# Kernel optimization log

Measured on AMD Instinct MI355X. Metric: run time of the kernel, lower is better.

The kernel has to match this reference:

```python
import jax, jax.numpy as jnp
import numpy as np

N = 128       # SSM state size
L = 32768     # l_max / sequence length
DT_MIN, DT_MAX = 0.001, 0.1


def setup_inputs() -> dict:
    key = jax.random.key(0)
    ku, ka, kb, kc, ks = jax.random.split(key, 5)
    u = jax.random.normal(ku, (L,), dtype=jnp.float32)
    # lecun_normal: std = 1/sqrt(fan_in); shift A by -2I for stability over L powers
    A = jax.random.normal(ka, (N, N), dtype=jnp.float32) * (1.0 / np.sqrt(N)) - 2.0 * jnp.eye(N, dtype=jnp.float32)
    B = jax.random.normal(kb, (N, 1), dtype=jnp.float32)            # fan_in=1 -> std 1
    C = jax.random.normal(kc, (1, N), dtype=jnp.float32) * (1.0 / np.sqrt(N))
    D = jnp.ones((1,), dtype=jnp.float32)
    log_step = jax.random.uniform(ks, (1,), dtype=jnp.float32) * (np.log(DT_MAX) - np.log(DT_MIN)) + np.log(DT_MIN)
    return {"u": u, "A": A, "B": B, "C": C, "D": D, "log_step": log_step}


def discretize(a, b, step):
    # bilinear (Tustin) discretization, identical to the flax module
    i = jnp.eye(a.shape[0], dtype=a.dtype)
    bl = jnp.linalg.inv(i - (step / 2.0) * a)
    ab = bl @ (i + (step / 2.0) * a)
    bb = (bl * step) @ b
    return ab, bb


def k_conv(ab, bb, cb, l):
    # K[t] = cb @ ab^t @ bb  -- same math as the matrix_power list-comp,
    # computed with a single scan carrying x_t = ab^t @ bb  (N,1)
    def step(x, _):
        k_t = (cb @ x).reshape(())
        return ab @ x, k_t
    _, k = jax.lax.scan(step, bb, None, length=l)
    return k  # (l,)


def causal_convolution(u, k):
    l = u.shape[0]
    ud = jnp.fft.rfft(jnp.pad(u, (0, k.shape[0])))
    kd = jnp.fft.rfft(jnp.pad(k, (0, l)))
    return jnp.fft.irfft(ud * kd)[:l]


def reference(u, A, B, C, D, log_step):
    step = jnp.exp(log_step)
    ab, bb = discretize(A, B, step)
    K = k_conv(ab, bb, C, u.shape[0])
    return causal_convolution(u, K) + D * u
```

## Files before the change

### kernel.cpp

```cpp
#include <hip/hip_runtime.h>
#include <math.h>

#define L_SEQ 32768
#define RSTR 136
#define PL   17408
#define GP   16384

typedef unsigned short u16;
typedef float f32x4 __attribute__((ext_vector_type(4)));
typedef short bf16x8 __attribute__((ext_vector_type(8)));
typedef u16 u16x4 __attribute__((ext_vector_type(4)));

__device__ __forceinline__ u16 f2bf(float x) {
  unsigned u = __float_as_uint(x);
  u = u + 0x7FFFu + ((u >> 16) & 1u);
  return (u16)(u >> 16);
}
__device__ __forceinline__ float bf2f(u16 h) {
  return __uint_as_float(((unsigned)h) << 16);
}
__device__ __forceinline__ int sg(int k) {
  return (k & 7) + ((k >> 5) << 3) + (((k >> 3) & 3) << 5);
}
__device__ __forceinline__ f32x4 MF(bf16x8 a, bf16x8 b, f32x4 c) {
  return __builtin_amdgcn_mfma_f32_16x16x32_bf16(a, b, c, 0, 0, 0);
}

template<int ASRC,int BSRC,int OUTM,int OUTG,int MODE>
__device__ void mm(u16* lds, const u16* gA, int aPl, const u16* gB, int bPl,
                   u16* gO, int oPl, int gOrow0, u16* gO2,
                   int Mrows, int N, float c3, const u16* gE, const u16* gEt) {
  u16* Mh = lds;          u16* Ml = lds + PL;
  u16* Th = lds + 2 * PL; u16* Tl = lds + 3 * PL;
  const int t = threadIdx.x, lane = t & 63;
  const int la = lane & 15, g = lane >> 4;
  const int w = t >> 6;
  const int r0 = (w >> 2) << 5, c0 = (w & 3) << 5;
  constexpr bool doA = (OUTM == 2) || (OUTG == 2) || (OUTG == 3);
  constexpr bool doT = (OUTM >= 1) || (OUTG == 1) || (OUTG == 3);
  const bool act = (r0 < Mrows) && (c0 < N);

  __syncthreads();

  f32x4 acc[2][2], accT[2][2];
#pragma unroll
  for (int i = 0; i < 2; ++i)
#pragma unroll
    for (int j = 0; j < 2; ++j) {
      acc[i][j] = (f32x4){0.f, 0.f, 0.f, 0.f};
      accT[i][j] = (f32x4){0.f, 0.f, 0.f, 0.f};
    }

  if (act) {
#pragma unroll
    for (int kb = 0; kb < 4; ++kb) {
      const int kp = (g << 5) + (kb << 3);
      bf16x8 Ah[2], Al[2], Bh[2], Bl[2];
#pragma unroll
      for (int fr = 0; fr < 2; ++fr) {
        const int ar = r0 + (fr << 4) + la;
        if constexpr (ASRC == 0) {
          Ah[fr] = *(const bf16x8*)(Mh + ar * RSTR + kp);
          Al[fr] = *(const bf16x8*)(Ml + ar * RSTR + kp);
        } else {
          Ah[fr] = *(const bf16x8*)(gA + ar * 128 + kp);
          Al[fr] = *(const bf16x8*)(gA + aPl + ar * 128 + kp);
        }
      }
#pragma unroll
      for (int fc = 0; fc < 2; ++fc) {
        const int bc = c0 + (fc << 4) + la;
        if constexpr (BSRC == 0) {
          Bh[fc] = *(const bf16x8*)(Th + bc * RSTR + kp);
          Bl[fc] = *(const bf16x8*)(Tl + bc * RSTR + kp);
        } else {
          Bh[fc] = *(const bf16x8*)(gB + bc * 128 + kp);
          Bl[fc] = *(const bf16x8*)(gB + bPl + bc * 128 + kp);
        }
      }
#pragma unroll
      for (int fr = 0; fr < 2; ++fr)
#pragma unroll
        for (int fc = 0; fc < 2; ++fc) {
          if constexpr (doA) {
            acc[fr][fc] = MF(Ah[fr], Bh[fc], acc[fr][fc]);
            acc[fr][fc] = MF(Ah[fr], Bl[fc], acc[fr][fc]);
            acc[fr][fc] = MF(Al[fr], Bh[fc], acc[fr][fc]);
          }
          if constexpr (doT) {
            accT[fr][fc] = MF(Bh[fc], Ah[fr], accT[fr][fc]);
            accT[fr][fc] = MF(Bh[fc], Al[fr], accT[fr][fc]);
            accT[fr][fc] = MF(Bl[fc], Ah[fr], accT[fr][fc]);
          }
        }
    }
  }

  __syncthreads();

  if (!act) return;

  if constexpr (doT) {
#pragma unroll
    for (int fr = 0; fr < 2; ++fr)
#pragma unroll
      for (int fc = 0; fc < 2; ++fc) {
        const int rr = r0 + (fr << 4) + la;
        const int cb = c0 + (fc << 4) + (g << 2);
        const int scb = sg(cb);
        float v[4];
#pragma unroll
        for (int j = 0; j < 4; ++j) v[j] = accT[fr][fc][j];
        if constexpr (MODE == 2) {
#pragma unroll
          for (int j = 0; j < 4; ++j)
            v[j] += bf2f(gE[rr * 128 + scb + j]) + bf2f(gE[GP + rr * 128 + scb + j])
                  + bf2f(Mh[rr * RSTR + scb + j]) + bf2f(Ml[rr * RSTR + scb + j])
                  + ((rr == cb + j) ? 1.f : 0.f);
        }
        if constexpr (MODE == 4) {
#pragma unroll
          for (int j = 0; j < 4; ++j)
            v[j] = c3 * (v[j] + bf2f(gE[rr * 128 + scb + j]) +
                         bf2f(gE[GP + rr * 128 + scb + j])) -
                   ((rr == cb + j) ? 1.f : 0.f);
        }
        u16x4 hi, lo;
#pragma unroll
        for (int j = 0; j < 4; ++j) {
          u16 h = f2bf(v[j]); hi[j] = h; lo[j] = f2bf(v[j] - bf2f(h));
        }
        if constexpr (OUTM == 2) {
          *(u16x4*)(Mh + rr * RSTR + scb) = hi;
          *(u16x4*)(Ml + rr * RSTR + scb) = lo;
        }
        if constexpr (OUTG == 1) {
          if (rr < Mrows) {
            *(u16x4*)(gO + (gOrow0 + rr) * 128 + scb) = hi;
            *(u16x4*)(gO + oPl + (gOrow0 + rr) * 128 + scb) = lo;
          }
        }
        if constexpr (OUTG == 3) {
          *(u16x4*)(gO + rr * 128 + scb) = hi;
          *(u16x4*)(gO + oPl + rr * 128 + scb) = lo;
        }
      }
  }
  if constexpr (doA) {
#pragma unroll
    for (int fr = 0; fr < 2; ++fr)
#pragma unroll
      for (int fc = 0; fc < 2; ++fc) {
        const int cc = c0 + (fc << 4) + la;
        const int rb = r0 + (fr << 4) + (g << 2);
        const int srb = sg(rb);
        float v[4];
#pragma unroll
        for (int j = 0; j < 4; ++j) v[j] = acc[fr][fc][j];
        if constexpr (MODE == 2) {
          const int scc = sg(cc);
#pragma unroll
          for (int j = 0; j < 4; ++j)
            v[j] += bf2f(gE[(rb + j) * 128 + scc]) + bf2f(gE[GP + (rb + j) * 128 + scc])
                  + bf2f(Th[cc * RSTR + srb + j]) + bf2f(Tl[cc * RSTR + srb + j])
                  + ((rb + j == cc) ? 1.f : 0.f);
        }
        if constexpr (MODE == 4) {
#pragma unroll
          for (int j = 0; j < 4; ++j)
            v[j] = c3 * (v[j] + bf2f(gEt[cc * 128 + srb + j]) +
                         bf2f(gEt[GP + cc * 128 + srb + j])) -
                   ((rb + j == cc) ? 1.f : 0.f);
        }
        u16x4 hi, lo;
#pragma unroll
        for (int j = 0; j < 4; ++j) {
          u16 h = f2bf(v[j]); hi[j] = h; lo[j] = f2bf(v[j] - bf2f(h));
        }
        if constexpr (OUTM == 2) {
          *(u16x4*)(Th + cc * RSTR + srb) = hi;
          *(u16x4*)(Tl + cc * RSTR + srb) = lo;
        }
        if constexpr (OUTG == 2) {
          if (cc < N) {
            *(u16x4*)(gO + (gOrow0 + cc) * 128 + srb) = hi;
            *(u16x4*)(gO + oPl + (gOrow0 + cc) * 128 + srb) = lo;
          }
        }
        if constexpr (OUTG == 3) {
          *(u16x4*)(gO2 + cc * 128 + srb) = hi;
          *(u16x4*)(gO2 + oPl + cc * 128 + srb) = lo;
        }
      }
  }
}

__global__ void __launch_bounds__(1024, 4) chain_k(const float* __restrict__ A,
                                                   const float* __restrict__ Bv,
                                                   const float* __restrict__ Cv,
                                                   const float* __restrict__ lstep,
                                                   u16* ws) {
  extern __shared__ u16 lds[];
  const int bid = blockIdx.x;
  u16* gT    = ws + bid * 131072;
  u16* gU12  = gT + 32768;
  u16* gU12t = gT + 65536;
  u16* rt = ws + 262144;
  u16* gs = ws + 327680;

  const int t = threadIdx.x;
  const float step = expf(lstep[0]);
  const float alpha = 0.5f * step / (1.f + step);
  const float c3 = 2.f / (1.f + step);
  u16* Mh = lds; u16* Ml = lds + PL; u16* Th = lds + 2 * PL; u16* Tl = lds + 3 * PL;

#pragma unroll
  for (int i = 0; i < 4; ++i) {
    int e4 = (t + (i << 10)) << 2;
    int r = e4 >> 7, c = e4 & 127;
    float4 av = *(const float4*)(A + e4);
    float vv[4] = {av.x, av.y, av.z, av.w};
    u16x4 hi, lo;
#pragma unroll
    for (int j = 0; j < 4; ++j) {
      float v = alpha * (vv[j] + ((r == c + j) ? 2.f : 0.f));
      u16 h = f2bf(v); hi[j] = h; lo[j] = f2bf(v - bf2f(h));
    }
    int sc = sg(c), sr = sg(r);
    *(u16x4*)(Mh + r * RSTR + sc) = hi;
    *(u16x4*)(Ml + r * RSTR + sc) = lo;
    *(u16x4*)(gT + r * 128 + sc) = hi;
    *(u16x4*)(gT + GP + r * 128 + sc) = lo;
#pragma unroll
    for (int j = 0; j < 4; ++j) {
      Th[(c + j) * RSTR + sr] = hi[j];
      Tl[(c + j) * RSTR + sr] = lo[j];
    }
  }

  mm<0,0,2,0,0>(lds, 0,0, 0,0, 0,0,0,0, 128,128, 0.f, 0,0);
  mm<1,0,0,3,2>(lds, gT,GP, 0,0, gU12,GP,0,gU12t, 128,128, 0.f, gT,0);
  mm<0,0,2,0,0>(lds, 0,0, 0,0, 0,0,0,0, 128,128, 0.f, 0,0);
  mm<1,0,2,0,4>(lds, gU12,GP, 0,0, 0,0,0,0, 128,128, c3, gU12,gU12t);

  if (bid == 0) {
    __syncthreads();
    if (t < 128) {
      float a2 = 0.f;
      for (int p = 0; p < 128; ++p)
        a2 = fmaf(bf2f(Mh[t * RSTR + p]) + bf2f(Ml[t * RSTR + p]), Bv[sg(p)], a2);
      float v = 0.5f * step * (a2 + Bv[t]);
      u16 h = f2bf(v);
      rt[sg(t)] = h;
      rt[32768 + sg(t)] = f2bf(v - bf2f(h));
    }
    for (int k = 0; k < 8; ++k) {
      mm<0,1,0,2,0>(lds, 0,0, rt,32768, rt,32768,(1<<k),0, 128,(1<<k), 0.f, 0,0);
      if (k < 7) mm<0,0,2,0,0>(lds, 0,0, 0,0, 0,0,0,0, 128,128, 0.f, 0,0);
    }
  } else {
    __syncthreads();
    if (t < 128) {
      float v = Cv[t];
      u16 h = f2bf(v);
      gs[sg(t)] = h;
      gs[GP + sg(t)] = f2bf(v - bf2f(h));
    }
    for (int k = 0; k < 8; ++k)
      mm<0,0,2,0,0>(lds, 0,0, 0,0, 0,0,0,0, 128,128, 0.f, 0,0);
    for (int k = 0; k < 7; ++k) {
      mm<1,0,0,1,0>(lds, gs,GP, 0,0, gs,GP,(1<<k),0, (1<<k),128, 0.f, 0,0);
      if (k < 6) mm<0,0,2,0,0>(lds, 0,0, 0,0, 0,0,0,0, 128,128, 0.f, 0,0);
    }
  }
}

__global__ __launch_bounds__(256) void kmat_k(const u16* __restrict__ gs,
                                              const u16* __restrict__ rt,
                                              float* __restrict__ Kv) {
  __shared__ float srow[128];
  int t1 = blockIdx.x, t0 = threadIdx.x;
  if (t0 < 128)
    srow[t0] = bf2f(gs[t1 * 128 + t0]) + bf2f(gs[GP + t1 * 128 + t0]);
  __syncthreads();
  const u16* rh = rt + t0 * 128;
  const u16* rl = rt + 32768 + t0 * 128;
  float acc = 0.f;
#pragma unroll 4
  for (int p = 0; p < 128; p += 8) {
    uint4 qh = *(const uint4*)(rh + p);
    uint4 ql = *(const uint4*)(rl + p);
    unsigned dh[4] = {qh.x, qh.y, qh.z, qh.w};
    unsigned dl[4] = {ql.x, ql.y, ql.z, ql.w};
#pragma unroll
    for (int j = 0; j < 4; ++j) {
      acc = fmaf(srow[p + 2 * j],     bf2f((u16)dh[j]) + bf2f((u16)dl[j]), acc);
      acc = fmaf(srow[p + 2 * j + 1],
                 bf2f((u16)(dh[j] >> 16)) + bf2f((u16)(dl[j] >> 16)), acc);
    }
  }
  Kv[t1 * 256 + t0] = acc;
}

__global__ __launch_bounds__(128) void conv_k(const float* __restrict__ u,
                                              const float* __restrict__ Kv,
                                              float* __restrict__ Pp) {
  __shared__ __align__(16) float ks[512];
  __shared__ __align__(16) float usw[1024];

  int bid = blockIdx.x, tid = threadIdx.x;
  int m = (int)((sqrtf(8.f * (float)bid + 1.f) - 1.f) * 0.5f);
  while ((m + 1) * (m + 2) / 2 <= bid) ++m;
  while (m * (m + 1) / 2 > bid) --m;
  int c = bid - m * (m + 1) / 2;
  int w0 = (m - c - 1) << 9;

  for (int idx = tid; idx < 512; idx += 128) ks[idx] = Kv[(c << 9) + idx];
  for (int idx = tid; idx < 1024; idx += 128) {
    int gi = w0 + idx;
    float v = (gi >= 0) ? u[gi] : 0.f;
    int b = idx >> 2;
    int pb = b ^ ((b >> 3) & 7);
    usw[(pb << 2) | (idx & 3)] = v;
  }
  __syncthreads();

  int tb = tid << 2;

#define LD4(x)                                                      \
  (*(const float4*)&usw[((((x) >> 2) ^ ((((x) >> 2) >> 3) & 7)) << 2)])

  float4 wlo = LD4(508 + tb);
  float4 whi = LD4(512 + tb);
  float acc0 = 0.f, acc1 = 0.f, acc2 = 0.f, acc3 = 0.f;

#pragma unroll 4
  for (int s8 = 0; s8 < 512; s8 += 4) {
    float4 k4 = *(const float4*)&ks[s8];
    acc0 = fmaf(k4.x, whi.x, acc0);
    acc0 = fmaf(k4.y, wlo.w, acc0);
    acc0 = fmaf(k4.z, wlo.z, acc0);
    acc0 = fmaf(k4.w, wlo.y, acc0);
    acc1 = fmaf(k4.x, whi.y, acc1);
    acc1 = fmaf(k4.y, whi.x, acc1);
    acc1 = fmaf(k4.z, wlo.w, acc1);
    acc1 = fmaf(k4.w, wlo.z, acc1);
    acc2 = fmaf(k4.x, whi.z, acc2);
    acc2 = fmaf(k4.y, whi.y, acc2);
    acc2 = fmaf(k4.z, whi.x, acc2);
    acc2 = fmaf(k4.w, wlo.w, acc2);
    acc3 = fmaf(k4.x, whi.w, acc3);
    acc3 = fmaf(k4.y, whi.z, acc3);
    acc3 = fmaf(k4.z, whi.y, acc3);
    acc3 = fmaf(k4.w, whi.x, acc3);
    if (s8 < 508) {
      whi = wlo;
      wlo = LD4(504 + tb - s8);
    }
  }
#undef LD4

  float* dst = Pp + (bid << 9) + tb;
  *(float4*)dst = make_float4(acc0, acc1, acc2, acc3);
}

__global__ __launch_bounds__(256) void reduce_k(const float* __restrict__ Pp,
                                                const float* __restrict__ u,
                                                const float* __restrict__ D,
                                                float* __restrict__ y) {
  int t = blockIdx.x * 256 + threadIdx.x;
  if (t >= L_SEQ) return;
  int m = t >> 9;
  int base = ((m * (m + 1) / 2) << 9) + (t & 511);
  float acc = D[0] * u[t];
  for (int c = 0; c <= m; ++c) acc += Pp[base + (c << 9)];
  y[t] = acc;
}

extern "C" void kernel_launch(void* const* d_in, const int* in_sizes, int n_in,
                              void* d_out, int out_size, void* d_ws, size_t ws_size,
                              hipStream_t stream) {
  (void)in_sizes; (void)n_in; (void)out_size; (void)ws_size;
  const float* u     = (const float*)d_in[0];
  const float* A     = (const float*)d_in[1];
  const float* B     = (const float*)d_in[2];
  const float* C     = (const float*)d_in[3];
  const float* D     = (const float*)d_in[4];
  const float* lstep = (const float*)d_in[5];
  float* y = (float*)d_out;
  u16* ws = (u16*)d_ws;

  u16* rt = ws + 262144;
  u16* gs = ws + 327680;
  float* Kv = (float*)((char*)d_ws + 720896);
  float* Pp = (float*)((char*)d_ws + 851968);

  (void)hipFuncSetAttribute((const void*)chain_k,
                            hipFuncAttributeMaxDynamicSharedMemorySize, 139264);
  hipLaunchKernelGGL(chain_k, dim3(2), dim3(1024), 139264, stream, A, B, C, lstep, ws);
  hipLaunchKernelGGL(kmat_k, dim3(128), dim3(256), 0, stream, gs, rt, Kv);
  hipLaunchKernelGGL(conv_k, dim3(2080), dim3(128), 0, stream, u, Kv, Pp);
  hipLaunchKernelGGL(reduce_k, dim3(L_SEQ / 256), dim3(256), 0, stream, Pp, u, D, y);
}
```

Baseline: 210.2 us.

## Swizzle LDS matrix layout, double-buffer MFMA operand loads, drop redundant barriers

The padded, k-permuted LDS layout (stride 136 with the sg permutation) is replaced by an unpadded 128-stride layout with an XOR swizzle, so the global buffers now use natural ordering and the LDS footprint shrinks. The K-loop now prefetches the next k-block's operand fragments into a second register set while the current MFMAs run. The post-accumulation barrier is skipped when the result is not written back to LDS. These target LDS bank conflicts and latency in the serial matrix-squaring chain, at the cost of more registers and a change to the k-index mapping that every consumer must match.

```diff
diff --git a/kernel.cpp b/kernel.cpp
--- a/kernel.cpp
+++ b/kernel.cpp
@@ -2,9 +2,8 @@
 #include <math.h>
 
 #define L_SEQ 32768
-#define RSTR 136
-#define PL   17408
-#define GP   16384
+#define PL 16384
+#define GP 16384
 
 typedef unsigned short u16;
 typedef float f32x4 __attribute__((ext_vector_type(4)));
@@ -19,8 +18,8 @@
 __device__ __forceinline__ float bf2f(u16 h) {
   return __uint_as_float(((unsigned)h) << 16);
 }
-__device__ __forceinline__ int sg(int k) {
-  return (k & 7) + ((k >> 5) << 3) + (((k >> 3) & 3) << 5);
+__device__ __forceinline__ int MIDX(int r, int c) {
+  return (r << 7) + (c ^ ((r & 7) << 3));
 }
 __device__ __forceinline__ f32x4 MF(bf16x8 a, bf16x8 b, f32x4 c) {
   return __builtin_amdgcn_mfma_f32_16x16x32_bf16(a, b, c, 0, 0, 0);
@@ -37,7 +36,7 @@
   const int w = t >> 6;
   const int r0 = (w >> 2) << 5, c0 = (w & 3) << 5;
   constexpr bool doA = (OUTM == 2) || (OUTG == 2) || (OUTG == 3);
-  constexpr bool doT = (OUTM >= 1) || (OUTG == 1) || (OUTG == 3);
+  constexpr bool doT = (OUTM == 2) || (OUTG == 1) || (OUTG == 3);
   const bool act = (r0 < Mrows) && (c0 < N);
 
   __syncthreads();
@@ -52,51 +51,56 @@
     }
 
   if (act) {
-#pragma unroll
-    for (int kb = 0; kb < 4; ++kb) {
-      const int kp = (g << 5) + (kb << 3);
-      bf16x8 Ah[2], Al[2], Bh[2], Bl[2];
+    bf16x8 Ah[2][2], Al[2][2], Bh[2][2], Bl[2][2];
+    auto load_stage = [&](int kb, int s) {
+      const int kp = (kb << 5) + (g << 3);
 #pragma unroll
       for (int fr = 0; fr < 2; ++fr) {
         const int ar = r0 + (fr << 4) + la;
         if constexpr (ASRC == 0) {
-          Ah[fr] = *(const bf16x8*)(Mh + ar * RSTR + kp);
-          Al[fr] = *(const bf16x8*)(Ml + ar * RSTR + kp);
+          Ah[s][fr] = *(const bf16x8*)(Mh + MIDX(ar, kp));
+          Al[s][fr] = *(const bf16x8*)(Ml + MIDX(ar, kp));
         } else {
-          Ah[fr] = *(const bf16x8*)(gA + ar * 128 + kp);
-          Al[fr] = *(const bf16x8*)(gA + aPl + ar * 128 + kp);
+          Ah[s][fr] = *(const bf16x8*)(gA + ar * 128 + kp);
+          Al[s][fr] = *(const bf16x8*)(gA + aPl + ar * 128 + kp);
         }
       }
 #pragma unroll
       for (int fc = 0; fc < 2; ++fc) {
         const int bc = c0 + (fc << 4) + la;
         if constexpr (BSRC == 0) {
-          Bh[fc] = *(const bf16x8*)(Th + bc * RSTR + kp);
-          Bl[fc] = *(const bf16x8*)(Tl + bc * RSTR + kp);
+          Bh[s][fc] = *(const bf16x8*)(Th + MIDX(bc, kp));
+          Bl[s][fc] = *(const bf16x8*)(Tl + MIDX(bc, kp));
         } else {
-          Bh[fc] = *(const bf16x8*)(gB + bc * 128 + kp);
-          Bl[fc] = *(const bf16x8*)(gB + bPl + bc * 128 + kp);
+          Bh[s][fc] = *(const bf16x8*)(gB + bc * 128 + kp);
+          Bl[s][fc] = *(const bf16x8*)(gB + bPl + bc * 128 + kp);
         }
       }
+    };
+    load_stage(0, 0);
+#pragma unroll
+    for (int kb = 0; kb < 4; ++kb) {
+      const int cur = kb & 1;
+      if (kb < 3) load_stage(kb + 1, cur ^ 1);
 #pragma unroll
       for (int fr = 0; fr < 2; ++fr)
 #pragma unroll
         for (int fc = 0; fc < 2; ++fc) {
           if constexpr (doA) {
-            acc[fr][fc] = MF(Ah[fr], Bh[fc], acc[fr][fc]);
-            acc[fr][fc] = MF(Ah[fr], Bl[fc], acc[fr][fc]);
-            acc[fr][fc] = MF(Al[fr], Bh[fc], acc[fr][fc]);
+            acc[fr][fc] = MF(Ah[cur][fr], Bh[cur][fc], acc[fr][fc]);
+            acc[fr][fc] = MF(Ah[cur][fr], Bl[cur][fc], acc[fr][fc]);
+            acc[fr][fc] = MF(Al[cur][fr], Bh[cur][fc], acc[fr][fc]);
           }
           if constexpr (doT) {
-            accT[fr][fc] = MF(Bh[fc], Ah[fr], accT[fr][fc]);
-            accT[fr][fc] = MF(Bh[fc], Al[fr], accT[fr][fc]);
-            accT[fr][fc] = MF(Bl[fc], Ah[fr], accT[fr][fc]);
+            accT[fr][fc] = MF(Bh[cur][fc], Ah[cur][fr], accT[fr][fc]);
+            accT[fr][fc] = MF(Bh[cur][fc], Al[cur][fr], accT[fr][fc]);
+            accT[fr][fc] = MF(Bl[cur][fc], Ah[cur][fr], accT[fr][fc]);
           }
         }
     }
   }
 
-  __syncthreads();
+  if constexpr (OUTM == 2) __syncthreads();
 
   if (!act) return;
 
@@ -107,22 +111,21 @@
       for (int fc = 0; fc < 2; ++fc) {
         const int rr = r0 + (fr << 4) + la;
         const int cb = c0 + (fc << 4) + (g << 2);
-        const int scb = sg(cb);
         float v[4];
 #pragma unroll
         for (int j = 0; j < 4; ++j) v[j] = accT[fr][fc][j];
         if constexpr (MODE == 2) {
 #pragma unroll
           for (int j = 0; j < 4; ++j)
-            v[j] += bf2f(gE[rr * 128 + scb + j]) + bf2f(gE[GP + rr * 128 + scb + j])
-                  + bf2f(Mh[rr * RSTR + scb + j]) + bf2f(Ml[rr * RSTR + scb + j])
+            v[j] += bf2f(gE[rr * 128 + cb + j]) + bf2f(gE[GP + rr * 128 + cb + j])
+                  + bf2f(Mh[MIDX(rr, cb + j)]) + bf2f(Ml[MIDX(rr, cb + j)])
                   + ((rr == cb + j) ? 1.f : 0.f);
         }
         if constexpr (MODE == 4) {
 #pragma unroll
           for (int j = 0; j < 4; ++j)
-            v[j] = c3 * (v[j] + bf2f(gE[rr * 128 + scb + j]) +
-                         bf2f(gE[GP + rr * 128 + scb + j])) -
+            v[j] = c3 * (v[j] + bf2f(gE[rr * 128 + cb + j]) +
+                         bf2f(gE[GP + rr * 128 + cb + j])) -
                    ((rr == cb + j) ? 1.f : 0.f);
         }
         u16x4 hi, lo;
@@ -131,18 +134,18 @@
           u16 h = f2bf(v[j]); hi[j] = h; lo[j] = f2bf(v[j] - bf2f(h));
         }
         if constexpr (OUTM == 2) {
-          *(u16x4*)(Mh + rr * RSTR + scb) = hi;
-          *(u16x4*)(Ml + rr * RSTR + scb) = lo;
+          *(u16x4*)(Mh + MIDX(rr, cb)) = hi;
+          *(u16x4*)(Ml + MIDX(rr, cb)) = lo;
         }
         if constexpr (OUTG == 1) {
           if (rr < Mrows) {
-            *(u16x4*)(gO + (gOrow0 + rr) * 128 + scb) = hi;
-            *(u16x4*)(gO + oPl + (gOrow0 + rr) * 128 + scb) = lo;
+            *(u16x4*)(gO + (gOrow0 + rr) * 128 + cb) = hi;
+            *(u16x4*)(gO + oPl + (gOrow0 + rr) * 128 + cb) = lo;
           }
         }
         if constexpr (OUTG == 3) {
-          *(u16x4*)(gO + rr * 128 + scb) = hi;
-          *(u16x4*)(gO + oPl + rr * 128 + scb) = lo;
+          *(u16x4*)(gO + rr * 128 + cb) = hi;
+          *(u16x4*)(gO + oPl + rr * 128 + cb) = lo;
         }
       }
   }
@@ -153,23 +156,21 @@
       for (int fc = 0; fc < 2; ++fc) {
         const int cc = c0 + (fc << 4) + la;
         const int rb = r0 + (fr << 4) + (g << 2);
-        const int srb = sg(rb);
         float v[4];
 #pragma unroll
         for (int j = 0; j < 4; ++j) v[j] = acc[fr][fc][j];
         if constexpr (MODE == 2) {
-          const int scc = sg(cc);
 #pragma unroll
           for (int j = 0; j < 4; ++j)
-            v[j] += bf2f(gE[(rb + j) * 128 + scc]) + bf2f(gE[GP + (rb + j) * 128 + scc])
-                  + bf2f(Th[cc * RSTR + srb + j]) + bf2f(Tl[cc * RSTR + srb + j])
+            v[j] += bf2f(gE[(rb + j) * 128 + cc]) + bf2f(gE[GP + (rb + j) * 128 + cc])
+                  + bf2f(Th[MIDX(cc, rb + j)]) + bf2f(Tl[MIDX(cc, rb + j)])
                   + ((rb + j == cc) ? 1.f : 0.f);
         }
         if constexpr (MODE == 4) {
 #pragma unroll
           for (int j = 0; j < 4; ++j)
-            v[j] = c3 * (v[j] + bf2f(gEt[cc * 128 + srb + j]) +
-                         bf2f(gEt[GP + cc * 128 + srb + j])) -
+            v[j] = c3 * (v[j] + bf2f(gEt[cc * 128 + rb + j]) +
+                         bf2f(gEt[GP + cc * 128 + rb + j])) -
                    ((rb + j == cc) ? 1.f : 0.f);
         }
         u16x4 hi, lo;
@@ -178,18 +179,18 @@
           u16 h = f2bf(v[j]); hi[j] = h; lo[j] = f2bf(v[j] - bf2f(h));
         }
         if constexpr (OUTM == 2) {
-          *(u16x4*)(Th + cc * RSTR + srb) = hi;
-          *(u16x4*)(Tl + cc * RSTR + srb) = lo;
+          *(u16x4*)(Th + MIDX(cc, rb)) = hi;
+          *(u16x4*)(Tl + MIDX(cc, rb)) = lo;
         }
         if constexpr (OUTG == 2) {
           if (cc < N) {
-            *(u16x4*)(gO + (gOrow0 + cc) * 128 + srb) = hi;
-            *(u16x4*)(gO + oPl + (gOrow0 + cc) * 128 + srb) = lo;
+            *(u16x4*)(gO + (gOrow0 + cc) * 128 + rb) = hi;
+            *(u16x4*)(gO + oPl + (gOrow0 + cc) * 128 + rb) = lo;
           }
         }
         if constexpr (OUTG == 3) {
-          *(u16x4*)(gO2 + cc * 128 + srb) = hi;
-          *(u16x4*)(gO2 + oPl + cc * 128 + srb) = lo;
+          *(u16x4*)(gO2 + cc * 128 + rb) = hi;
+          *(u16x4*)(gO2 + oPl + cc * 128 + rb) = lo;
         }
       }
   }
@@ -226,15 +227,14 @@
       float v = alpha * (vv[j] + ((r == c + j) ? 2.f : 0.f));
       u16 h = f2bf(v); hi[j] = h; lo[j] = f2bf(v - bf2f(h));
     }
-    int sc = sg(c), sr = sg(r);
-    *(u16x4*)(Mh + r * RSTR + sc) = hi;
-    *(u16x4*)(Ml + r * RSTR + sc) = lo;
-    *(u16x4*)(gT + r * 128 + sc) = hi;
-    *(u16x4*)(gT + GP + r * 128 + sc) = lo;
+    *(u16x4*)(Mh + MIDX(r, c)) = hi;
+    *(u16x4*)(Ml + MIDX(r, c)) = lo;
+    *(u16x4*)(gT + r * 128 + c) = hi;
+    *(u16x4*)(gT + GP + r * 128 + c) = lo;
 #pragma unroll
     for (int j = 0; j < 4; ++j) {
-      Th[(c + j) * RSTR + sr] = hi[j];
-      Tl[(c + j) * RSTR + sr] = lo[j];
+      Th[MIDX(c + j, r)] = hi[j];
+      Tl[MIDX(c + j, r)] = lo[j];
     }
   }
 
@@ -248,11 +248,11 @@
     if (t < 128) {
       float a2 = 0.f;
       for (int p = 0; p < 128; ++p)
-        a2 = fmaf(bf2f(Mh[t * RSTR + p]) + bf2f(Ml[t * RSTR + p]), Bv[sg(p)], a2);
+        a2 = fmaf(bf2f(Mh[MIDX(t, p)]) + bf2f(Ml[MIDX(t, p)]), Bv[p], a2);
       float v = 0.5f * step * (a2 + Bv[t]);
       u16 h = f2bf(v);
-      rt[sg(t)] = h;
-      rt[32768 + sg(t)] = f2bf(v - bf2f(h));
+      rt[t] = h;
+      rt[32768 + t] = f2bf(v - bf2f(h));
     }
     for (int k = 0; k < 8; ++k) {
       mm<0,1,0,2,0>(lds, 0,0, rt,32768, rt,32768,(1<<k),0, 128,(1<<k), 0.f, 0,0);
@@ -263,8 +263,8 @@
     if (t < 128) {
       float v = Cv[t];
       u16 h = f2bf(v);
-      gs[sg(t)] = h;
-      gs[GP + sg(t)] = f2bf(v - bf2f(h));
+      gs[t] = h;
+      gs[GP + t] = f2bf(v - bf2f(h));
     }
     for (int k = 0; k < 8; ++k)
       mm<0,0,2,0,0>(lds, 0,0, 0,0, 0,0,0,0, 128,128, 0.f, 0,0);
@@ -396,8 +396,8 @@
   float* Pp = (float*)((char*)d_ws + 851968);
 
   (void)hipFuncSetAttribute((const void*)chain_k,
-                            hipFuncAttributeMaxDynamicSharedMemorySize, 139264);
-  hipLaunchKernelGGL(chain_k, dim3(2), dim3(1024), 139264, stream, A, B, C, lstep, ws);
+                            hipFuncAttributeMaxDynamicSharedMemorySize, 131072);
+  hipLaunchKernelGGL(chain_k, dim3(2), dim3(1024), 131072, stream, A, B, C, lstep, ws);
   hipLaunchKernelGGL(kmat_k, dim3(128), dim3(256), 0, stream, gs, rt, Kv);
   hipLaunchKernelGGL(conv_k, dim3(2080), dim3(128), 0, stream, u, Kv, Pp);
   hipLaunchKernelGGL(reduce_k, dim3(L_SEQ / 256), dim3(256), 0, stream, Pp, u, D, y);
```

Measured after the change: 214.2 us. Within noise of the previous version (+1.9%).
